# Kernel optimization log

Measured on AMD Instinct MI355X. Metric: run time of the kernel, lower is better.

Reference implementation:

```python
import jax, jax.numpy as jnp
import numpy as np

N, C, F = 16384, 2048, 512


def setup_inputs() -> dict:
    key = jax.random.key(0)
    kx, km = jax.random.split(key)
    x = jax.random.normal(kx, (N, F), dtype=jnp.float32)
    means = jax.random.normal(km, (C, F), dtype=jnp.float32)
    return {"x": x, "means": means}


def reference(x, means):
    # Negative Euclidean distance scores: -sqrt(sum_f (x[n,f] - means[c,f])^2)
    # intermediate the naive expand/pow/sum formulation materializes).
    x_sq = jnp.sum(x * x, axis=-1, keepdims=True)          # [N, 1]
    m_sq = jnp.sum(means * means, axis=-1)                 # [C]
    cross = jnp.einsum('nf,cf->nc', x, means)              # [N, C]
    d2 = jnp.maximum(x_sq + m_sq[None, :] - 2.0 * cross, 0.0)
    return -jnp.sqrt(d2)
```

## Files before the change

kernel.cpp:

```cpp
#include <hip/hip_runtime.h>
#include <hip/hip_bf16.h>

constexpr int N_ROWS = 16384;
constexpr int C_CLS  = 2048;
constexpr int F_DIM  = 512;

typedef __bf16 bf16x8 __attribute__((ext_vector_type(8)));
typedef float  f32x16 __attribute__((ext_vector_type(16)));

__global__ __launch_bounds__(256) void prep_rows(
    const float* __restrict__ x,
    const float* __restrict__ means,
    __hip_bfloat162* __restrict__ xb,
    __hip_bfloat162* __restrict__ mb,
    float* __restrict__ xsq,
    float* __restrict__ msq)
{
    int row = blockIdx.x;
    const float* src;
    __hip_bfloat162* dst;
    float* sq;
    if (row < N_ROWS) { src = x; dst = xb; sq = xsq; }
    else { row -= N_ROWS; src = means; dst = mb; sq = msq; }

    const int tid = threadIdx.x;
    const float2 v = ((const float2*)(src + (size_t)row * F_DIM))[tid];

    __hip_bfloat162 p;
    p.x = __float2bfloat16(v.x);
    p.y = __float2bfloat16(v.y);
    dst[(size_t)row * (F_DIM / 2) + tid] = p;

    float ss = v.x * v.x + v.y * v.y;
    #pragma unroll
    for (int off = 32; off > 0; off >>= 1) ss += __shfl_down(ss, off);

    __shared__ float red[4];
    if ((tid & 63) == 0) red[tid >> 6] = ss;
    __syncthreads();
    if (tid == 0) sq[row] = red[0] + red[1] + red[2] + red[3];
}

__device__ __forceinline__ void async_copy16(const __hip_bfloat16* g,
                                             __hip_bfloat16* l)
{
    __builtin_amdgcn_global_load_lds(
        (const __attribute__((address_space(1))) unsigned int*)g,
        (__attribute__((address_space(3))) unsigned int*)l,
        16, 0, 0);
}

__global__ __launch_bounds__(256) void ncm_gemm(
    const __hip_bfloat16* __restrict__ xb,
    const __hip_bfloat16* __restrict__ mb,
    const float* __restrict__ xsq,
    const float* __restrict__ msq,
    float* __restrict__ out)
{
    constexpr int BM = 128, BK = 64, NKT = F_DIM / BK;

    __shared__ alignas(16) __hip_bfloat16 sA[2][BM * BK];

    const int tid  = threadIdx.x;
    const int wave = tid >> 6;
    const int lane = tid & 63;
    const int wm   = wave >> 1;
    const int wn   = wave & 1;

    const int row0 = blockIdx.y * BM;
    const int col0 = blockIdx.x * 128;

    const int srow   = lane >> 3;
    const int schunk = (lane & 7) ^ srow;
    const __hip_bfloat16* gA =
        xb + (size_t)(row0 + wave * 32 + srow) * F_DIM + schunk * 8;

    const int lrow  = lane & 31;
    const int khalf = lane >> 5;
    const __hip_bfloat16* gB =
        mb + (size_t)(col0 + wn * 64 + lrow) * F_DIM + khalf * 8;

    f32x16 acc[2][2] = {};

    #pragma unroll
    for (int i = 0; i < 4; ++i)
        async_copy16(gA + (size_t)i * 8 * F_DIM,
                     &sA[0][(wave * 32 + i * 8) * BK]);

    for (int kt = 0; kt < NKT; ++kt) {
        const int p = kt & 1;
        __syncthreads();

        if (kt + 1 < NKT) {
            const int k0n = (kt + 1) * BK;
            #pragma unroll
            for (int i = 0; i < 4; ++i)
                async_copy16(gA + (size_t)i * 8 * F_DIM + k0n,
                             &sA[1 - p][(wave * 32 + i * 8) * BK]);
        }

        bf16x8 bfr[4][2];
        #pragma unroll
        for (int s = 0; s < 4; ++s)
            #pragma unroll
            for (int nt = 0; nt < 2; ++nt)
                bfr[s][nt] = *(const bf16x8*)
                    (gB + (size_t)nt * 32 * F_DIM + kt * BK + s * 16);

        #pragma unroll
        for (int s = 0; s < 4; ++s) {
            const int pos = ((2 * s + khalf) ^ (lane & 7)) * 8;
            bf16x8 af[2];
            #pragma unroll
            for (int mt = 0; mt < 2; ++mt)
                af[mt] = *(const bf16x8*)
                    &sA[p][(wm * 64 + mt * 32 + lrow) * BK + pos];
            #pragma unroll
            for (int mt = 0; mt < 2; ++mt)
                #pragma unroll
                for (int nt = 0; nt < 2; ++nt)
                    acc[mt][nt] = __builtin_amdgcn_mfma_f32_32x32x16_bf16(
                        af[mt], bfr[s][nt], acc[mt][nt], 0, 0, 0);
        }
    }

    #pragma unroll
    for (int mt = 0; mt < 2; ++mt) {
        const int rbase = row0 + wm * 64 + mt * 32 + 4 * khalf;
        float xs[16];
        #pragma unroll
        for (int r = 0; r < 16; ++r)
            xs[r] = xsq[rbase + (r & 3) + 8 * (r >> 2)];
        #pragma unroll
        for (int nt = 0; nt < 2; ++nt) {
            const int col = col0 + wn * 64 + nt * 32 + lrow;
            const float ms = msq[col];
            #pragma unroll
            for (int r = 0; r < 16; ++r) {
                const int row = rbase + (r & 3) + 8 * (r >> 2);
                const float d2 =
                    fmaxf(xs[r] + ms - 2.0f * acc[mt][nt][r], 0.0f);
                out[(size_t)row * C_CLS + col] = -sqrtf(d2);
            }
        }
    }
}

extern "C" void kernel_launch(void* const* d_in, const int* in_sizes, int n_in,
                              void* d_out, int out_size, void* d_ws,
                              size_t ws_size, hipStream_t stream)
{
    const float* x     = (const float*)d_in[0];
    const float* means = (const float*)d_in[1];
    float* out = (float*)d_out;

    char* ws = (char*)d_ws;
    __hip_bfloat16* xb = (__hip_bfloat16*)ws;
    __hip_bfloat16* mb = (__hip_bfloat16*)(ws + (size_t)N_ROWS * F_DIM * 2);
    float* xsq = (float*)(ws + (size_t)(N_ROWS + C_CLS) * F_DIM * 2);
    float* msq = xsq + N_ROWS;

    prep_rows<<<N_ROWS + C_CLS, 256, 0, stream>>>(
        x, means, (__hip_bfloat162*)xb, (__hip_bfloat162*)mb, xsq, msq);

    dim3 grid(C_CLS / 128, N_ROWS / 128);
    ncm_gemm<<<grid, 256, 0, stream>>>(xb, mb, xsq, msq, out);
}
```

Measured before the change: 227.8 us.

## Use 256x256 tiles with both operands staged in LDS and transposed float4 stores

The GEMM tile grows from 128x128 to 256x256 with 512 threads (8 waves). Both the means and x tiles are now staged in LDS through async global-to-LDS copies, where before B fragments were read straight from global memory on every k-step. Operands are swapped (means on the M side, x on the N side) so each lane's accumulator entries are consecutive classes, which lets the epilogue write float4 stores. This raises data reuse and cuts global traffic, but it also raises register pressure (8 accumulators per wave) and LDS use (128 KB per block), which may limit occupancy.

```diff
diff --git a/kernel.cpp b/kernel.cpp
--- a/kernel.cpp
+++ b/kernel.cpp
@@ -50,42 +50,46 @@
         16, 0, 0);
 }
 
-__global__ __launch_bounds__(256) void ncm_gemm(
+__global__ __launch_bounds__(512, 2) void ncm_gemm(
     const __hip_bfloat16* __restrict__ xb,
     const __hip_bfloat16* __restrict__ mb,
     const float* __restrict__ xsq,
     const float* __restrict__ msq,
     float* __restrict__ out)
 {
-    constexpr int BM = 128, BK = 64, NKT = F_DIM / BK;
+    constexpr int BC = 256, BN = 256, BK = 64, NKT = F_DIM / BK;
 
-    __shared__ alignas(16) __hip_bfloat16 sA[2][BM * BK];
+    __shared__ alignas(16) __hip_bfloat16 sM[2][BC * BK];
+    __shared__ alignas(16) __hip_bfloat16 sX[2][BN * BK];
 
     const int tid  = threadIdx.x;
     const int wave = tid >> 6;
     const int lane = tid & 63;
-    const int wm   = wave >> 1;
+    const int wc   = wave >> 1;
     const int wn   = wave & 1;
 
-    const int row0 = blockIdx.y * BM;
-    const int col0 = blockIdx.x * 128;
+    const int c0 = blockIdx.x * BC;
+    const int n0 = blockIdx.y * BN;
 
     const int srow   = lane >> 3;
     const int schunk = (lane & 7) ^ srow;
-    const __hip_bfloat16* gA =
-        xb + (size_t)(row0 + wave * 32 + srow) * F_DIM + schunk * 8;
+    const bool stA   = (wave < 4);
+    const int  sw    = wave & 3;
+    const __hip_bfloat16* gsrc = stA
+        ? mb + (size_t)(c0 + sw * 64 + srow) * F_DIM + schunk * 8
+        : xb + (size_t)(n0 + sw * 64 + srow) * F_DIM + schunk * 8;
+    __hip_bfloat16* ldst[2] = {
+        stA ? &sM[0][sw * 64 * BK] : &sX[0][sw * 64 * BK],
+        stA ? &sM[1][sw * 64 * BK] : &sX[1][sw * 64 * BK] };
+
+    f32x16 acc[2][4] = {};
 
     const int lrow  = lane & 31;
     const int khalf = lane >> 5;
-    const __hip_bfloat16* gB =
-        mb + (size_t)(col0 + wn * 64 + lrow) * F_DIM + khalf * 8;
-
-    f32x16 acc[2][2] = {};
 
     #pragma unroll
-    for (int i = 0; i < 4; ++i)
-        async_copy16(gA + (size_t)i * 8 * F_DIM,
-                     &sA[0][(wave * 32 + i * 8) * BK]);
+    for (int i = 0; i < 8; ++i)
+        async_copy16(gsrc + (size_t)i * 8 * F_DIM, ldst[0] + i * 8 * BK);
 
     for (int kt = 0; kt < NKT; ++kt) {
         const int p = kt & 1;
@@ -93,54 +97,55 @@
 
         if (kt + 1 < NKT) {
             const int k0n = (kt + 1) * BK;
+            __hip_bfloat16* ld = ldst[1 - p];
             #pragma unroll
-            for (int i = 0; i < 4; ++i)
-                async_copy16(gA + (size_t)i * 8 * F_DIM + k0n,
-                             &sA[1 - p][(wave * 32 + i * 8) * BK]);
+            for (int i = 0; i < 8; ++i)
+                async_copy16(gsrc + (size_t)i * 8 * F_DIM + k0n,
+                             ld + i * 8 * BK);
         }
-
-        bf16x8 bfr[4][2];
-        #pragma unroll
-        for (int s = 0; s < 4; ++s)
-            #pragma unroll
-            for (int nt = 0; nt < 2; ++nt)
-                bfr[s][nt] = *(const bf16x8*)
-                    (gB + (size_t)nt * 32 * F_DIM + kt * BK + s * 16);
 
         #pragma unroll
         for (int s = 0; s < 4; ++s) {
             const int pos = ((2 * s + khalf) ^ (lane & 7)) * 8;
-            bf16x8 af[2];
+            bf16x8 mf[2], xf[4];
             #pragma unroll
-            for (int mt = 0; mt < 2; ++mt)
-                af[mt] = *(const bf16x8*)
-                    &sA[p][(wm * 64 + mt * 32 + lrow) * BK + pos];
+            for (int ct = 0; ct < 2; ++ct)
+                mf[ct] = *(const bf16x8*)
+                    &sM[p][(wc * 64 + ct * 32 + lrow) * BK + pos];
             #pragma unroll
-            for (int mt = 0; mt < 2; ++mt)
+            for (int nt = 0; nt < 4; ++nt)
+                xf[nt] = *(const bf16x8*)
+                    &sX[p][(wn * 128 + nt * 32 + lrow) * BK + pos];
+            #pragma unroll
+            for (int ct = 0; ct < 2; ++ct)
                 #pragma unroll
-                for (int nt = 0; nt < 2; ++nt)
-                    acc[mt][nt] = __builtin_amdgcn_mfma_f32_32x32x16_bf16(
-                        af[mt], bfr[s][nt], acc[mt][nt], 0, 0, 0);
+                for (int nt = 0; nt < 4; ++nt)
+                    acc[ct][nt] = __builtin_amdgcn_mfma_f32_32x32x16_bf16(
+                        mf[ct], xf[nt], acc[ct][nt], 0, 0, 0);
         }
     }
 
+    float xq[4];
     #pragma unroll
-    for (int mt = 0; mt < 2; ++mt) {
-        const int rbase = row0 + wm * 64 + mt * 32 + 4 * khalf;
-        float xs[16];
+    for (int nt = 0; nt < 4; ++nt)
+        xq[nt] = xsq[n0 + wn * 128 + nt * 32 + lrow];
+
+    #pragma unroll
+    for (int ct = 0; ct < 2; ++ct) {
+        const int cb = c0 + wc * 64 + ct * 32 + 4 * khalf;
         #pragma unroll
-        for (int r = 0; r < 16; ++r)
-            xs[r] = xsq[rbase + (r & 3) + 8 * (r >> 2)];
-        #pragma unroll
-        for (int nt = 0; nt < 2; ++nt) {
-            const int col = col0 + wn * 64 + nt * 32 + lrow;
-            const float ms = msq[col];
+        for (int g = 0; g < 4; ++g) {
+            const int cg = cb + 8 * g;
+            const float4 mq = *(const float4*)&msq[cg];
             #pragma unroll
-            for (int r = 0; r < 16; ++r) {
-                const int row = rbase + (r & 3) + 8 * (r >> 2);
-                const float d2 =
-                    fmaxf(xs[r] + ms - 2.0f * acc[mt][nt][r], 0.0f);
-                out[(size_t)row * C_CLS + col] = -sqrtf(d2);
+            for (int nt = 0; nt < 4; ++nt) {
+                const int n = n0 + wn * 128 + nt * 32 + lrow;
+                float4 o;
+                o.x = -sqrtf(fmaxf(xq[nt] + mq.x - 2.0f * acc[ct][nt][4*g+0], 0.0f));
+                o.y = -sqrtf(fmaxf(xq[nt] + mq.y - 2.0f * acc[ct][nt][4*g+1], 0.0f));
+                o.z = -sqrtf(fmaxf(xq[nt] + mq.z - 2.0f * acc[ct][nt][4*g+2], 0.0f));
+                o.w = -sqrtf(fmaxf(xq[nt] + mq.w - 2.0f * acc[ct][nt][4*g+3], 0.0f));
+                *(float4*)&out[(size_t)n * C_CLS + cg] = o;
             }
         }
     }
@@ -163,6 +168,6 @@
     prep_rows<<<N_ROWS + C_CLS, 256, 0, stream>>>(
         x, means, (__hip_bfloat162*)xb, (__hip_bfloat162*)mb, xsq, msq);
 
-    dim3 grid(C_CLS / 128, N_ROWS / 128);
-    ncm_gemm<<<grid, 256, 0, stream>>>(xb, mb, xsq, msq, out);
+    dim3 grid(C_CLS / 256, N_ROWS / 256);
+    ncm_gemm<<<grid, 512, 0, stream>>>(xb, mb, xsq, msq, out);
 }
```

New measurement: 254.8 us. +11.8%, slower.
